# Kernel optimization log

Hardware: AMD Instinct MI355X
Metric: run time of the kernel (lower is better)

Reference implementation:

```python
import jax, jax.numpy as jnp
import numpy as np

B, L, C, H, WS = 8, 1024, 1024, 16, 128  # batch, seq (grid 32x32), dim, heads, window_size
HD = C // H


def _local_mask(seq_len, window_size):
    # blocked where |i - j| > window_size // 2 (matches create_local_attention_mask)
    idx = jnp.arange(seq_len)
    return jnp.abs(idx[:, None] - idx[None, :]) > window_size // 2  # True = blocked


def setup_inputs() -> dict:
    key = jax.random.key(0)
    k0, k1, k2 = jax.random.split(key, 3)
    x = jax.random.normal(k0, (B, L, C), jnp.float32)
    in_proj_w = jax.random.normal(k1, (3 * C, C), jnp.float32) * 0.02
    in_proj_b = jnp.zeros((3 * C,), jnp.float32)
    out_w = jax.random.normal(k2, (C, C), jnp.float32) * 0.02
    out_b = jnp.zeros((C,), jnp.float32)
    return {"x": x, "in_proj_w": in_proj_w, "in_proj_b": in_proj_b,
            "out_w": out_w, "out_b": out_b}


def reference(x, in_proj_w, in_proj_b, out_w, out_b):
    # nn.MultiheadAttention (batch_first, self-attention) with boolean attn_mask.
    Bc, Lc, Cc = x.shape
    qkv = x @ in_proj_w.T + in_proj_b              # [B, L, 3C]
    q, k, v = jnp.split(qkv, 3, axis=-1)
    to_heads = lambda t: t.reshape(Bc, Lc, H, HD).transpose(0, 2, 1, 3)  # [B,H,L,hd]
    q, k, v = to_heads(q), to_heads(k), to_heads(v)
    scale = 1.0 / np.sqrt(HD).astype(np.float32)
    scores = jnp.einsum('bhqd,bhkd->bhqk', q, k) * scale  # [B,H,L,L]
    blocked = _local_mask(Lc, WS)
    scores = jnp.where(blocked[None, None], -jnp.inf, scores)
    attn = jax.nn.softmax(scores, axis=-1)
    out = jnp.einsum('bhqk,bhkd->bhqd', attn, v)           # [B,H,L,hd]
    out = out.transpose(0, 2, 1, 3).reshape(Bc, Lc, Cc)
    return out @ out_w.T + out_b
```

## Files before the change

### kernel.cpp

```cpp
#include <hip/hip_runtime.h>
#include <hip/hip_bf16.h>
#include <stdint.h>


typedef __attribute__((ext_vector_type(8))) short bf16x8;
typedef __attribute__((ext_vector_type(4))) float f32x4;

__device__ inline unsigned short f2b(float f) {
    __hip_bfloat16 h = __float2bfloat16(f);
    return *reinterpret_cast<unsigned short*>(&h);
}

__device__ inline void gld16(const unsigned short* g, unsigned short* l) {
    __builtin_amdgcn_global_load_lds(
        (const __attribute__((address_space(1))) void*)g,
        (__attribute__((address_space(3))) void*)l, 16, 0, 0);
}

#define BM 128
#define BN 128
#define BK 64

__global__ void __launch_bounds__(256) cast_inputs(
    const float4* __restrict__ x, const float4* __restrict__ w1,
    const float4* __restrict__ w2,
    uint4* __restrict__ xb, uint4* __restrict__ w1b, uint4* __restrict__ w2b)
{
    const int P0 = 1048576, P1 = 393216, P2 = 131072;
    int stride = gridDim.x * blockDim.x;
    for (int i = blockIdx.x * blockDim.x + threadIdx.x; i < P0 + P1 + P2; i += stride) {
        const float4* src; uint4* dst; int idx;
        if (i < P0)           { src = x;  dst = xb;  idx = i; }
        else if (i < P0 + P1) { src = w1; dst = w1b; idx = i - P0; }
        else                  { src = w2; dst = w2b; idx = i - P0 - P1; }
        float4 a = src[idx * 2], b = src[idx * 2 + 1];
        unsigned short t[8] = {f2b(a.x), f2b(a.y), f2b(a.z), f2b(a.w),
                               f2b(b.x), f2b(b.y), f2b(b.z), f2b(b.w)};
        dst[idx] = *(uint4*)t;
    }
}

__global__ void __launch_bounds__(256) gemm_qkv(
    const unsigned short* __restrict__ A,
    const unsigned short* __restrict__ W,
    const float* __restrict__ bias,
    unsigned short* __restrict__ Qo,
    unsigned short* __restrict__ Ko,
    unsigned short* __restrict__ Vo)
{
    const int K = 1024;
    int n0 = blockIdx.x * BN;
    int m0 = blockIdx.y * BM;
    int tid = threadIdx.x;
    int wave = tid >> 6, lane = tid & 63;
    int lm = lane & 15, quad = lane >> 4;
    int mblk = (wave & 1) * 64, nblk = (wave >> 1) * 64;

    __shared__ unsigned short As[BM * BK];
    __shared__ unsigned short Bs[BN * BK];

    int drow = lane >> 3;
    int gcc  = (lane & 7) ^ drow;
    const unsigned short* ga[4]; const unsigned short* gb[4];
    unsigned short *la[4], *lb[4];
#pragma unroll
    for (int p = 0; p < 4; ++p) {
        int r = wave * 32 + p * 8 + drow;
        ga[p] = A + (size_t)(m0 + r) * K + gcc * 8;
        gb[p] = W + (size_t)(n0 + r) * K + gcc * 8;
        la[p] = As + (wave * 32 + p * 8) * 64;
        lb[p] = Bs + (wave * 32 + p * 8) * 64;
    }
    int lm7 = lm & 7;

    f32x4 acc[4][4];
#pragma unroll
    for (int i = 0; i < 4; ++i)
#pragma unroll
        for (int j = 0; j < 4; ++j)
            acc[i][j] = (f32x4){0.f, 0.f, 0.f, 0.f};

    for (int k0 = 0; k0 < K; k0 += BK) {
        __syncthreads();
#pragma unroll
        for (int p = 0; p < 4; ++p) gld16(ga[p] + k0, la[p]);
#pragma unroll
        for (int p = 0; p < 4; ++p) gld16(gb[p] + k0, lb[p]);
        __syncthreads();
        bf16x8 af[4][2], bfr[4][2];
#pragma unroll
        for (int i = 0; i < 4; ++i)
#pragma unroll
            for (int hhh = 0; hhh < 2; ++hhh)
                af[i][hhh] = *(const bf16x8*)(As + (mblk + i * 16 + lm) * 64 +
                                              (((hhh * 4 + quad) ^ lm7) << 3));
#pragma unroll
        for (int j = 0; j < 4; ++j)
#pragma unroll
            for (int hhh = 0; hhh < 2; ++hhh)
                bfr[j][hhh] = *(const bf16x8*)(Bs + (nblk + j * 16 + lm) * 64 +
                                               (((hhh * 4 + quad) ^ lm7) << 3));
#pragma unroll
        for (int i = 0; i < 4; ++i)
#pragma unroll
            for (int j = 0; j < 4; ++j) {
                acc[i][j] = __builtin_amdgcn_mfma_f32_16x16x32_bf16(af[i][0], bfr[j][0], acc[i][j], 0, 0, 0);
                acc[i][j] = __builtin_amdgcn_mfma_f32_16x16x32_bf16(af[i][1], bfr[j][1], acc[i][j], 0, 0, 0);
            }
    }

#pragma unroll
    for (int j = 0; j < 4; ++j) {
        int n = n0 + nblk + j * 16 + lm;
        float bv = bias[n];
        int sec = n >> 10, rem = n & 1023;
        int h = rem >> 6, d = rem & 63;
        unsigned short* dst = (sec == 0) ? Qo : (sec == 1) ? Ko : Vo;
#pragma unroll
        for (int i = 0; i < 4; ++i) {
#pragma unroll
            for (int r = 0; r < 4; ++r) {
                int m = m0 + mblk + i * 16 + quad * 4 + r;
                int bb = m >> 10, sl = m & 1023;
                size_t idx = ((size_t)((bb * 16 + h) * 1024 + sl)) * 64 + d;
                dst[idx] = f2b(acc[i][j][r] + bv);
            }
        }
    }
}

__global__ void __launch_bounds__(256) attn_local(
    const unsigned short* __restrict__ Qg,
    const unsigned short* __restrict__ Kg,
    const unsigned short* __restrict__ Vg,
    unsigned short* __restrict__ Og)
{
    const int KP = 72;
    const int VP = 200;
    __shared__ unsigned short Ks[192 * KP];
    __shared__ unsigned short Vt[64 * VP];

    int tid = threadIdx.x;
    int wave = tid >> 6, lane = tid & 63;
    int lm = lane & 15, quad = lane >> 4;

    int bh = blockIdx.x >> 4;
    int qt = blockIdx.x & 15;
    int q0 = qt * 64;
    int b = bh >> 4, h = bh & 15;
    const unsigned short* Qbh = Qg + (size_t)bh * 1024 * 64;
    const unsigned short* Kbh = Kg + (size_t)bh * 1024 * 64;
    const unsigned short* Vbh = Vg + (size_t)bh * 1024 * 64;
    int j0 = q0 - 64;

#pragma unroll
    for (int it = 0; it < 6; ++it) {
        int id = it * 256 + tid;
        int r = id >> 3;
        int c = (id & 7) * 8;
        int j = j0 + r;
        uint4 kv, vv;
        kv.x = kv.y = kv.z = kv.w = 0;
        vv = kv;
        if (j >= 0 && j < 1024) {
            kv = *(const uint4*)(Kbh + (size_t)j * 64 + c);
            vv = *(const uint4*)(Vbh + (size_t)j * 64 + c);
        }
        *(uint4*)(Ks + r * KP + c) = kv;
        unsigned short tmp[8];
        *(uint4*)tmp = vv;
#pragma unroll
        for (int e = 0; e < 8; ++e) Vt[(c + e) * VP + r] = tmp[e];
    }
    __syncthreads();

    int qrow = q0 + wave * 16;
    bf16x8 qf0 = *(const bf16x8*)(Qbh + (size_t)(qrow + lm) * 64 + quad * 8);
    bf16x8 qf1 = *(const bf16x8*)(Qbh + (size_t)(qrow + lm) * 64 + 32 + quad * 8);

    f32x4 sc[9];
#pragma unroll
    for (int kt = 0; kt < 9; ++kt) {
        int akt = wave + kt;
        f32x4 a = (f32x4){0.f, 0.f, 0.f, 0.f};
        bf16x8 k0f = *(const bf16x8*)(Ks + (akt * 16 + lm) * KP + quad * 8);
        bf16x8 k1f = *(const bf16x8*)(Ks + (akt * 16 + lm) * KP + 32 + quad * 8);
        a = __builtin_amdgcn_mfma_f32_16x16x32_bf16(qf0, k0f, a, 0, 0, 0);
        a = __builtin_amdgcn_mfma_f32_16x16x32_bf16(qf1, k1f, a, 0, 0, 0);
        sc[kt] = a;
    }

    float mx[4] = {-3e38f, -3e38f, -3e38f, -3e38f};
#pragma unroll
    for (int kt = 0; kt < 9; ++kt) {
        int jg = j0 + (wave + kt) * 16 + lm;
#pragma unroll
        for (int r = 0; r < 4; ++r) {
            int irow = q0 + wave * 16 + quad * 4 + r;
            int diff = irow - jg;
            bool ok = (jg >= 0) && (jg < 1024) && (diff <= 64) && (diff >= -64);
            float s = ok ? sc[kt][r] * 0.125f : -30000.0f;
            sc[kt][r] = s;
            mx[r] = fmaxf(mx[r], s);
        }
    }
#pragma unroll
    for (int off = 1; off <= 8; off <<= 1)
#pragma unroll
        for (int r = 0; r < 4; ++r)
            mx[r] = fmaxf(mx[r], __shfl_xor(mx[r], off, 64));

    float sum[4] = {0.f, 0.f, 0.f, 0.f};
#pragma unroll
    for (int kt = 0; kt < 9; ++kt)
#pragma unroll
        for (int r = 0; r < 4; ++r) {
            float p = __expf(sc[kt][r] - mx[r]);
            sc[kt][r] = p;
            sum[r] += p;
        }
#pragma unroll
    for (int off = 1; off <= 8; off <<= 1)
#pragma unroll
        for (int r = 0; r < 4; ++r)
            sum[r] += __shfl_xor(sum[r], off, 64);

    __syncthreads();
    unsigned short* Pb = Ks + wave * 3200;
#pragma unroll
    for (int kt = 0; kt < 9; ++kt) {
        int akt = wave + kt;
#pragma unroll
        for (int r = 0; r < 4; ++r)
            Pb[(quad * 4 + r) * VP + akt * 16 + lm] = f2b(sc[kt][r]);
    }
    {
        int zkt = (wave & 1) ? (wave - 1) : (wave + 9);
#pragma unroll
        for (int r = 0; r < 4; ++r)
            Pb[(quad * 4 + r) * VP + zkt * 16 + lm] = 0;
    }
    __syncthreads();

    int jclo = wave >> 1;
    f32x4 o[4];
#pragma unroll
    for (int n = 0; n < 4; ++n) o[n] = (f32x4){0.f, 0.f, 0.f, 0.f};
#pragma unroll
    for (int jc2 = 0; jc2 < 5; ++jc2) {
        int jc = jclo + jc2;
        bf16x8 pf = *(const bf16x8*)(Pb + lm * VP + jc * 32 + quad * 8);
#pragma unroll
        for (int n = 0; n < 4; ++n) {
            bf16x8 vf = *(const bf16x8*)(Vt + (n * 16 + lm) * VP + jc * 32 + quad * 8);
            o[n] = __builtin_amdgcn_mfma_f32_16x16x32_bf16(pf, vf, o[n], 0, 0, 0);
        }
    }

    float inv[4];
#pragma unroll
    for (int r = 0; r < 4; ++r) inv[r] = 1.0f / sum[r];
#pragma unroll
    for (int n = 0; n < 4; ++n)
#pragma unroll
        for (int r = 0; r < 4; ++r) {
            int orow = q0 + wave * 16 + quad * 4 + r;
            size_t oidx = ((size_t)(b * 1024 + orow)) * 1024 + h * 64 + n * 16 + lm;
            Og[oidx] = f2b(o[n][r] * inv[r]);
        }
}

__global__ void __launch_bounds__(256) gemm_proj(
    const unsigned short* __restrict__ A,
    const unsigned short* __restrict__ W,
    const float* __restrict__ bias,
    float* __restrict__ Out)
{
    const int K = 1024;
    int n0 = blockIdx.x * BN;
    int m0 = blockIdx.y * BM;
    int tid = threadIdx.x;
    int wave = tid >> 6, lane = tid & 63;
    int lm = lane & 15, quad = lane >> 4;
    int mblk = (wave & 1) * 64, nblk = (wave >> 1) * 64;

    __shared__ unsigned short As[BM * BK];
    __shared__ unsigned short Bs[BN * BK];

    int drow = lane >> 3;
    int gcc  = (lane & 7) ^ drow;
    const unsigned short* ga[4]; const unsigned short* gb[4];
    unsigned short *la[4], *lb[4];
#pragma unroll
    for (int p = 0; p < 4; ++p) {
        int r = wave * 32 + p * 8 + drow;
        ga[p] = A + (size_t)(m0 + r) * K + gcc * 8;
        gb[p] = W + (size_t)(n0 + r) * K + gcc * 8;
        la[p] = As + (wave * 32 + p * 8) * 64;
        lb[p] = Bs + (wave * 32 + p * 8) * 64;
    }
    int lm7 = lm & 7;

    f32x4 acc[4][4];
#pragma unroll
    for (int i = 0; i < 4; ++i)
#pragma unroll
        for (int j = 0; j < 4; ++j)
            acc[i][j] = (f32x4){0.f, 0.f, 0.f, 0.f};

    for (int k0 = 0; k0 < K; k0 += BK) {
        __syncthreads();
#pragma unroll
        for (int p = 0; p < 4; ++p) gld16(ga[p] + k0, la[p]);
#pragma unroll
        for (int p = 0; p < 4; ++p) gld16(gb[p] + k0, lb[p]);
        __syncthreads();
        bf16x8 af[4][2], bfr[4][2];
#pragma unroll
        for (int i = 0; i < 4; ++i)
#pragma unroll
            for (int hhh = 0; hhh < 2; ++hhh)
                af[i][hhh] = *(const bf16x8*)(As + (mblk + i * 16 + lm) * 64 +
                                              (((hhh * 4 + quad) ^ lm7) << 3));
#pragma unroll
        for (int j = 0; j < 4; ++j)
#pragma unroll
            for (int hhh = 0; hhh < 2; ++hhh)
                bfr[j][hhh] = *(const bf16x8*)(Bs + (nblk + j * 16 + lm) * 64 +
                                               (((hhh * 4 + quad) ^ lm7) << 3));
#pragma unroll
        for (int i = 0; i < 4; ++i)
#pragma unroll
            for (int j = 0; j < 4; ++j) {
                acc[i][j] = __builtin_amdgcn_mfma_f32_16x16x32_bf16(af[i][0], bfr[j][0], acc[i][j], 0, 0, 0);
                acc[i][j] = __builtin_amdgcn_mfma_f32_16x16x32_bf16(af[i][1], bfr[j][1], acc[i][j], 0, 0, 0);
            }
    }

#pragma unroll
    for (int j = 0; j < 4; ++j) {
        int n = n0 + nblk + j * 16 + lm;
        float bv = bias[n];
#pragma unroll
        for (int i = 0; i < 4; ++i) {
#pragma unroll
            for (int r = 0; r < 4; ++r) {
                int m = m0 + mblk + i * 16 + quad * 4 + r;
                Out[(size_t)m * 1024 + n] = acc[i][j][r] + bv;
            }
        }
    }
}

extern "C" void kernel_launch(void* const* d_in, const int* in_sizes, int n_in,
                              void* d_out, int out_size, void* d_ws, size_t ws_size,
                              hipStream_t stream) {
    const float* x  = (const float*)d_in[0];
    const float* w1 = (const float*)d_in[1];
    const float* b1 = (const float*)d_in[2];
    const float* w2 = (const float*)d_in[3];
    const float* b2 = (const float*)d_in[4];
    float* out = (float*)d_out;

    char* ws = (char*)d_ws;
    const size_t MB = 1024 * 1024;
    unsigned short* xb   = (unsigned short*)(ws);
    unsigned short* w1b  = (unsigned short*)(ws + 16 * MB);
    unsigned short* w2b  = (unsigned short*)(ws + 22 * MB);
    unsigned short* q    = (unsigned short*)(ws + 24 * MB);
    unsigned short* k    = (unsigned short*)(ws + 40 * MB);
    unsigned short* v    = (unsigned short*)d_out;
    unsigned short* attn = (unsigned short*)(ws);

    dim3 blk(256);
    cast_inputs<<<1536, blk, 0, stream>>>(
        (const float4*)x, (const float4*)w1, (const float4*)w2,
        (uint4*)xb, (uint4*)w1b, (uint4*)w2b);
    gemm_qkv<<<dim3(24, 64), blk, 0, stream>>>(xb, w1b, b1, q, k, v);
    attn_local<<<dim3(2048), blk, 0, stream>>>(q, k, v, attn);
    gemm_proj<<<dim3(8, 64), blk, 0, stream>>>(attn, w2b, b2, out);
}
```

Measured before the change: 210.0 us.

## Replace QKV and projection GEMMs with 8-wave double-buffered ping-pong GEMM template

```diff
diff --git a/kernel.cpp b/kernel.cpp
--- a/kernel.cpp
+++ b/kernel.cpp
@@ -16,10 +16,6 @@
         (const __attribute__((address_space(1))) void*)g,
         (__attribute__((address_space(3))) void*)l, 16, 0, 0);
 }
-
-#define BM 128
-#define BN 128
-#define BK 64
 
 __global__ void __launch_bounds__(256) cast_inputs(
     const float4* __restrict__ x, const float4* __restrict__ w1,
@@ -40,90 +36,167 @@
     }
 }
 
-__global__ void __launch_bounds__(256) gemm_qkv(
+
+#define STAGE_A(BUF, HM, T) do {                                              \
+    const int rbA = (HM) * 128 + wave * 8;                                    \
+    gld16(Aeff + (size_t)(rbA + drow) * 1024 + (T) * 64 + gcc * 8,            \
+          &As[BUF][rbA * 64]);                                                \
+    gld16(Aeff + (size_t)(rbA + 64 + drow) * 1024 + (T) * 64 + gcc * 8,       \
+          &As[BUF][(rbA + 64) * 64]);                                         \
+} while (0)
+
+#define STAGE_B(BUF, HN, T) do {                                              \
+    const int rbB = (HN) * (BN_T / 2) + wave * 8;                             \
+    gld16(Weff + (size_t)(rbB + drow) * 1024 + (T) * 64 + gcc * 8,            \
+          &Bs[BUF][rbB * 64]);                                                \
+    if constexpr (BN_T == 256) {                                              \
+        gld16(Weff + (size_t)(rbB + 64 + drow) * 1024 + (T) * 64 + gcc * 8,   \
+              &Bs[BUF][(rbB + 64) * 64]);                                     \
+    }                                                                         \
+} while (0)
+
+#define PH_READS(BUF, QM, QN) do {                                            \
+    _Pragma("unroll")                                                         \
+    for (int f = 0; f < 4; ++f) {                                             \
+        const int ar = ((QM) * 128 + f * 32 + wm * 16 + lm) * 64;             \
+        pa[f][0] = *(const bf16x8*)&As[BUF][ar + ((quad ^ lm7) << 3)];        \
+        pa[f][1] = *(const bf16x8*)&As[BUF][ar + (((4 + quad) ^ lm7) << 3)];  \
+    }                                                                         \
+    _Pragma("unroll")                                                         \
+    for (int g = 0; g < NGQ; ++g) {                                           \
+        const int br = (((QN) * NGQ + g) * 64 + wn * 16 + lm) * 64;           \
+        pb[g][0] = *(const bf16x8*)&Bs[BUF][br + ((quad ^ lm7) << 3)];        \
+        pb[g][1] = *(const bf16x8*)&Bs[BUF][br + (((4 + quad) ^ lm7) << 3)];  \
+    }                                                                         \
+} while (0)
+
+#define PH_MMA(QM, QN) do {                                                   \
+    __builtin_amdgcn_s_barrier();                                             \
+    asm volatile("s_waitcnt lgkmcnt(0)" ::: "memory");                        \
+    __builtin_amdgcn_sched_barrier(0);                                        \
+    __builtin_amdgcn_s_setprio(1);                                            \
+    _Pragma("unroll")                                                         \
+    for (int f = 0; f < 4; ++f) {                                             \
+        _Pragma("unroll")                                                     \
+        for (int g = 0; g < NGQ; ++g) {                                       \
+            acc[(QM)*4+f][(QN)*NGQ+g] = __builtin_amdgcn_mfma_f32_16x16x32_bf16( \
+                pa[f][0], pb[g][0], acc[(QM)*4+f][(QN)*NGQ+g], 0, 0, 0);      \
+            acc[(QM)*4+f][(QN)*NGQ+g] = __builtin_amdgcn_mfma_f32_16x16x32_bf16( \
+                pa[f][1], pb[g][1], acc[(QM)*4+f][(QN)*NGQ+g], 0, 0, 0);      \
+        }                                                                     \
+    }                                                                         \
+    __builtin_amdgcn_s_setprio(0);                                            \
+    __builtin_amdgcn_s_barrier();                                             \
+} while (0)
+
+#define VM_WAIT_STEADY do {                                                   \
+    if constexpr (BN_T == 256) { asm volatile("s_waitcnt vmcnt(4)" ::: "memory"); } \
+    else                       { asm volatile("s_waitcnt vmcnt(3)" ::: "memory"); } \
+} while (0)
+
+#define GROUP(BUF, T) do {                                                    \
+    PH_READS(BUF, 0, 0); if ((T) + 1 < NT) STAGE_A((BUF)^1, 1, (T)+1); PH_MMA(0, 0); \
+    PH_READS(BUF, 1, 0); if ((T) + 1 < NT) STAGE_B((BUF)^1, 1, (T)+1); PH_MMA(1, 0); \
+    PH_READS(BUF, 0, 1); if ((T) + 2 < NT) STAGE_B(BUF, 0, (T)+2);     PH_MMA(0, 1); \
+    PH_READS(BUF, 1, 1); if ((T) + 2 < NT) STAGE_A(BUF, 0, (T)+2);            \
+    if ((T) + 2 < NT) { VM_WAIT_STEADY; }                                     \
+    else { asm volatile("s_waitcnt vmcnt(0)" ::: "memory"); }                 \
+    PH_MMA(1, 1);                                                             \
+} while (0)
+
+template<int BN_T, bool SCATTER>
+__global__ void __launch_bounds__(512) gemm8p(
     const unsigned short* __restrict__ A,
     const unsigned short* __restrict__ W,
     const float* __restrict__ bias,
     unsigned short* __restrict__ Qo,
     unsigned short* __restrict__ Ko,
-    unsigned short* __restrict__ Vo)
+    unsigned short* __restrict__ Vo,
+    float* __restrict__ Out)
 {
-    const int K = 1024;
-    int n0 = blockIdx.x * BN;
-    int m0 = blockIdx.y * BM;
-    int tid = threadIdx.x;
-    int wave = tid >> 6, lane = tid & 63;
-    int lm = lane & 15, quad = lane >> 4;
-    int mblk = (wave & 1) * 64, nblk = (wave >> 1) * 64;
-
-    __shared__ unsigned short As[BM * BK];
-    __shared__ unsigned short Bs[BN * BK];
-
-    int drow = lane >> 3;
-    int gcc  = (lane & 7) ^ drow;
-    const unsigned short* ga[4]; const unsigned short* gb[4];
-    unsigned short *la[4], *lb[4];
-#pragma unroll
-    for (int p = 0; p < 4; ++p) {
-        int r = wave * 32 + p * 8 + drow;
-        ga[p] = A + (size_t)(m0 + r) * K + gcc * 8;
-        gb[p] = W + (size_t)(n0 + r) * K + gcc * 8;
-        la[p] = As + (wave * 32 + p * 8) * 64;
-        lb[p] = Bs + (wave * 32 + p * 8) * 64;
-    }
-    int lm7 = lm & 7;
-
-    f32x4 acc[4][4];
-#pragma unroll
-    for (int i = 0; i < 4; ++i)
-#pragma unroll
-        for (int j = 0; j < 4; ++j)
-            acc[i][j] = (f32x4){0.f, 0.f, 0.f, 0.f};
-
-    for (int k0 = 0; k0 < K; k0 += BK) {
-        __syncthreads();
-#pragma unroll
-        for (int p = 0; p < 4; ++p) gld16(ga[p] + k0, la[p]);
-#pragma unroll
-        for (int p = 0; p < 4; ++p) gld16(gb[p] + k0, lb[p]);
-        __syncthreads();
-        bf16x8 af[4][2], bfr[4][2];
-#pragma unroll
-        for (int i = 0; i < 4; ++i)
-#pragma unroll
-            for (int hhh = 0; hhh < 2; ++hhh)
-                af[i][hhh] = *(const bf16x8*)(As + (mblk + i * 16 + lm) * 64 +
-                                              (((hhh * 4 + quad) ^ lm7) << 3));
-#pragma unroll
-        for (int j = 0; j < 4; ++j)
-#pragma unroll
-            for (int hhh = 0; hhh < 2; ++hhh)
-                bfr[j][hhh] = *(const bf16x8*)(Bs + (nblk + j * 16 + lm) * 64 +
-                                               (((hhh * 4 + quad) ^ lm7) << 3));
-#pragma unroll
-        for (int i = 0; i < 4; ++i)
-#pragma unroll
-            for (int j = 0; j < 4; ++j) {
-                acc[i][j] = __builtin_amdgcn_mfma_f32_16x16x32_bf16(af[i][0], bfr[j][0], acc[i][j], 0, 0, 0);
-                acc[i][j] = __builtin_amdgcn_mfma_f32_16x16x32_bf16(af[i][1], bfr[j][1], acc[i][j], 0, 0, 0);
+    constexpr int NT  = 16;
+    constexpr int NFN = BN_T / 64;
+    constexpr int NGQ = NFN / 2;
+    constexpr int NDIM = SCATTER ? 3072 : 1024;
+    constexpr int NBX = NDIM / BN_T;
+    constexpr int QC  = (NBX * 32) / 8;
+
+    __shared__ unsigned short As[2][256 * 64];
+    __shared__ unsigned short Bs[2][BN_T * 64];
+
+    const int tid  = threadIdx.x;
+    const int wave = tid >> 6, lane = tid & 63;
+    const int wm = wave >> 2, wn = wave & 3;
+    const int lm = lane & 15, quad = lane >> 4;
+    const int lm7 = lm & 7;
+    const int drow = lane >> 3;
+    const int gcc  = (lane & 7) ^ drow;
+
+    const int id  = blockIdx.y * NBX + blockIdx.x;
+    const int swz = (id & 7) * QC + (id >> 3);
+    const int bx = swz % NBX, by = swz / NBX;
+    const int m0 = by * 256, n0 = bx * BN_T;
+
+    const unsigned short* Aeff = A + (size_t)m0 * 1024;
+    const unsigned short* Weff = W + (size_t)n0 * 1024;
+
+    f32x4 acc[8][NFN];
+#pragma unroll
+    for (int f = 0; f < 8; ++f)
+#pragma unroll
+        for (int g = 0; g < NFN; ++g)
+            acc[f][g] = (f32x4){0.f, 0.f, 0.f, 0.f};
+
+    bf16x8 pa[4][2];
+    bf16x8 pb[NGQ][2];
+
+    STAGE_A(0, 0, 0);
+    STAGE_A(0, 1, 0);
+    STAGE_B(0, 0, 0);
+    STAGE_B(0, 1, 0);
+    STAGE_B(1, 0, 1);
+    STAGE_A(1, 0, 1);
+    VM_WAIT_STEADY;
+    __builtin_amdgcn_s_barrier();
+
+#pragma unroll 1
+    for (int tp = 0; tp < NT / 2; ++tp) {
+        const int te = 2 * tp;
+        GROUP(0, te);
+        GROUP(1, te + 1);
+    }
+
+    if constexpr (SCATTER) {
+#pragma unroll
+        for (int g = 0; g < NFN; ++g) {
+            int n = n0 + g * 64 + wn * 16 + lm;
+            float bv = bias[n];
+            int sec = n >> 10, rem = n & 1023;
+            int h = rem >> 6, d = rem & 63;
+            unsigned short* dst = (sec == 0) ? Qo : (sec == 1) ? Ko : Vo;
+#pragma unroll
+            for (int f = 0; f < 8; ++f) {
+#pragma unroll
+                for (int r = 0; r < 4; ++r) {
+                    int m = m0 + f * 32 + wm * 16 + quad * 4 + r;
+                    int bb = m >> 10, sl = m & 1023;
+                    size_t idx = ((size_t)((bb * 16 + h) * 1024 + sl)) * 64 + d;
+                    dst[idx] = f2b(acc[f][g][r] + bv);
+                }
             }
-    }
-
-#pragma unroll
-    for (int j = 0; j < 4; ++j) {
-        int n = n0 + nblk + j * 16 + lm;
-        float bv = bias[n];
-        int sec = n >> 10, rem = n & 1023;
-        int h = rem >> 6, d = rem & 63;
-        unsigned short* dst = (sec == 0) ? Qo : (sec == 1) ? Ko : Vo;
-#pragma unroll
-        for (int i = 0; i < 4; ++i) {
-#pragma unroll
-            for (int r = 0; r < 4; ++r) {
-                int m = m0 + mblk + i * 16 + quad * 4 + r;
-                int bb = m >> 10, sl = m & 1023;
-                size_t idx = ((size_t)((bb * 16 + h) * 1024 + sl)) * 64 + d;
-                dst[idx] = f2b(acc[i][j][r] + bv);
+        }
+    } else {
+#pragma unroll
+        for (int g = 0; g < NFN; ++g) {
+            int n = n0 + g * 64 + wn * 16 + lm;
+            float bv = bias[n];
+#pragma unroll
+            for (int f = 0; f < 8; ++f) {
+#pragma unroll
+                for (int r = 0; r < 4; ++r) {
+                    int m = m0 + f * 32 + wm * 16 + quad * 4 + r;
+                    Out[(size_t)m * 1024 + n] = acc[f][g][r] + bv;
+                }
             }
         }
     }
@@ -270,88 +343,6 @@
         }
 }
 
-__global__ void __launch_bounds__(256) gemm_proj(
-    const unsigned short* __restrict__ A,
-    const unsigned short* __restrict__ W,
-    const float* __restrict__ bias,
-    float* __restrict__ Out)
-{
-    const int K = 1024;
-    int n0 = blockIdx.x * BN;
-    int m0 = blockIdx.y * BM;
-    int tid = threadIdx.x;
-    int wave = tid >> 6, lane = tid & 63;
-    int lm = lane & 15, quad = lane >> 4;
-    int mblk = (wave & 1) * 64, nblk = (wave >> 1) * 64;
-
-    __shared__ unsigned short As[BM * BK];
-    __shared__ unsigned short Bs[BN * BK];
-
-    int drow = lane >> 3;
-    int gcc  = (lane & 7) ^ drow;
-    const unsigned short* ga[4]; const unsigned short* gb[4];
-    unsigned short *la[4], *lb[4];
-#pragma unroll
-    for (int p = 0; p < 4; ++p) {
-        int r = wave * 32 + p * 8 + drow;
-        ga[p] = A + (size_t)(m0 + r) * K + gcc * 8;
-        gb[p] = W + (size_t)(n0 + r) * K + gcc * 8;
-        la[p] = As + (wave * 32 + p * 8) * 64;
-        lb[p] = Bs + (wave * 32 + p * 8) * 64;
-    }
-    int lm7 = lm & 7;
-
-    f32x4 acc[4][4];
-#pragma unroll
-    for (int i = 0; i < 4; ++i)
-#pragma unroll
-        for (int j = 0; j < 4; ++j)
-            acc[i][j] = (f32x4){0.f, 0.f, 0.f, 0.f};
-
-    for (int k0 = 0; k0 < K; k0 += BK) {
-        __syncthreads();
-#pragma unroll
-        for (int p = 0; p < 4; ++p) gld16(ga[p] + k0, la[p]);
-#pragma unroll
-        for (int p = 0; p < 4; ++p) gld16(gb[p] + k0, lb[p]);
-        __syncthreads();
-        bf16x8 af[4][2], bfr[4][2];
-#pragma unroll
-        for (int i = 0; i < 4; ++i)
-#pragma unroll
-            for (int hhh = 0; hhh < 2; ++hhh)
-                af[i][hhh] = *(const bf16x8*)(As + (mblk + i * 16 + lm) * 64 +
-                                              (((hhh * 4 + quad) ^ lm7) << 3));
-#pragma unroll
-        for (int j = 0; j < 4; ++j)
-#pragma unroll
-            for (int hhh = 0; hhh < 2; ++hhh)
-                bfr[j][hhh] = *(const bf16x8*)(Bs + (nblk + j * 16 + lm) * 64 +
-                                               (((hhh * 4 + quad) ^ lm7) << 3));
-#pragma unroll
-        for (int i = 0; i < 4; ++i)
-#pragma unroll
-            for (int j = 0; j < 4; ++j) {
-                acc[i][j] = __builtin_amdgcn_mfma_f32_16x16x32_bf16(af[i][0], bfr[j][0], acc[i][j], 0, 0, 0);
-                acc[i][j] = __builtin_amdgcn_mfma_f32_16x16x32_bf16(af[i][1], bfr[j][1], acc[i][j], 0, 0, 0);
-            }
-    }
-
-#pragma unroll
-    for (int j = 0; j < 4; ++j) {
-        int n = n0 + nblk + j * 16 + lm;
-        float bv = bias[n];
-#pragma unroll
-        for (int i = 0; i < 4; ++i) {
-#pragma unroll
-            for (int r = 0; r < 4; ++r) {
-                int m = m0 + mblk + i * 16 + quad * 4 + r;
-                Out[(size_t)m * 1024 + n] = acc[i][j][r] + bv;
-            }
-        }
-    }
-}
-
 extern "C" void kernel_launch(void* const* d_in, const int* in_sizes, int n_in,
                               void* d_out, int out_size, void* d_ws, size_t ws_size,
                               hipStream_t stream) {
@@ -372,11 +363,12 @@
     unsigned short* v    = (unsigned short*)d_out;
     unsigned short* attn = (unsigned short*)(ws);
 
-    dim3 blk(256);
-    cast_inputs<<<1536, blk, 0, stream>>>(
+    cast_inputs<<<1536, dim3(256), 0, stream>>>(
         (const float4*)x, (const float4*)w1, (const float4*)w2,
         (uint4*)xb, (uint4*)w1b, (uint4*)w2b);
-    gemm_qkv<<<dim3(24, 64), blk, 0, stream>>>(xb, w1b, b1, q, k, v);
-    attn_local<<<dim3(2048), blk, 0, stream>>>(q, k, v, attn);
-    gemm_proj<<<dim3(8, 64), blk, 0, stream>>>(attn, w2b, b2, out);
-}
+    gemm8p<256, true><<<dim3(12, 32), dim3(512), 0, stream>>>(
+        xb, w1b, b1, q, k, v, nullptr);
+    attn_local<<<dim3(2048), dim3(256), 0, stream>>>(q, k, v, attn);
+    gemm8p<128, false><<<dim3(8, 32), dim3(512), 0, stream>>>(
+        attn, w2b, b2, nullptr, nullptr, nullptr, out);
+}
```

New measurement: 235.7 us. 12.2% more time.

## Double-buffer GEMM LDS tiles, prefetch next tile during MFMA, add XCD workgroup swizzle

Applied to the files above, without the earlier changes.

```diff
diff --git a/kernel.cpp b/kernel.cpp
--- a/kernel.cpp
+++ b/kernel.cpp
@@ -40,36 +40,83 @@
     }
 }
 
-__global__ void __launch_bounds__(256) gemm_qkv(
+
+#define STG(BUF, T) do {                                                      \
+    _Pragma("unroll")                                                         \
+    for (int p = 0; p < 4; ++p) {                                             \
+        gld16(ga[p] + (T) * 64, &As[BUF][(wave * 32 + p * 8) * 64]);          \
+        gld16(gb[p] + (T) * 64, &Bs[BUF][(wave * 32 + p * 8) * 64]);          \
+    } } while (0)
+
+#define RDS(BUF) do {                                                         \
+    _Pragma("unroll")                                                         \
+    for (int i = 0; i < 4; ++i) {                                             \
+        _Pragma("unroll")                                                     \
+        for (int h = 0; h < 2; ++h) {                                         \
+            af[i][h]  = *(const bf16x8*)&As[BUF][(mblk + i * 16 + lm) * 64 +  \
+                                                 (((h * 4 + quad) ^ lm7) << 3)]; \
+            bfr[i][h] = *(const bf16x8*)&Bs[BUF][(nblk + i * 16 + lm) * 64 +  \
+                                                 (((h * 4 + quad) ^ lm7) << 3)]; \
+        }                                                                     \
+    } } while (0)
+
+#define MMA do {                                                              \
+    asm volatile("s_waitcnt lgkmcnt(0)" ::: "memory");                        \
+    __builtin_amdgcn_sched_barrier(0);                                        \
+    _Pragma("unroll")                                                         \
+    for (int i = 0; i < 4; ++i) {                                             \
+        _Pragma("unroll")                                                     \
+        for (int j = 0; j < 4; ++j) {                                         \
+            acc[i][j] = __builtin_amdgcn_mfma_f32_16x16x32_bf16(              \
+                af[i][0], bfr[j][0], acc[i][j], 0, 0, 0);                     \
+            acc[i][j] = __builtin_amdgcn_mfma_f32_16x16x32_bf16(              \
+                af[i][1], bfr[j][1], acc[i][j], 0, 0, 0);                     \
+        }                                                                     \
+    } } while (0)
+
+#define ITER(BUF, T) do {                                                     \
+    RDS(BUF);                                                                 \
+    STG(1 - (BUF), (T) + 1);                                                  \
+    MMA;                                                                      \
+    asm volatile("s_waitcnt vmcnt(0)" ::: "memory");                          \
+    __builtin_amdgcn_s_barrier();                                             \
+} while (0)
+
+template<bool SCATTER>
+__global__ void __launch_bounds__(256) gemm2p(
     const unsigned short* __restrict__ A,
     const unsigned short* __restrict__ W,
     const float* __restrict__ bias,
     unsigned short* __restrict__ Qo,
     unsigned short* __restrict__ Ko,
-    unsigned short* __restrict__ Vo)
+    unsigned short* __restrict__ Vo,
+    float* __restrict__ Out,
+    int NBX)
 {
     const int K = 1024;
-    int n0 = blockIdx.x * BN;
-    int m0 = blockIdx.y * BM;
     int tid = threadIdx.x;
     int wave = tid >> 6, lane = tid & 63;
     int lm = lane & 15, quad = lane >> 4;
     int mblk = (wave & 1) * 64, nblk = (wave >> 1) * 64;
 
-    __shared__ unsigned short As[BM * BK];
-    __shared__ unsigned short Bs[BN * BK];
+    int nwg = NBX * 64;
+    int id  = blockIdx.y * NBX + blockIdx.x;
+    int cpx = nwg >> 3;
+    int swz = (id & 7) * cpx + (id >> 3);
+    int bx = swz % NBX, by = swz / NBX;
+    int n0 = bx * BN, m0 = by * BM;
+
+    __shared__ unsigned short As[2][BM * BK];
+    __shared__ unsigned short Bs[2][BN * BK];
 
     int drow = lane >> 3;
     int gcc  = (lane & 7) ^ drow;
     const unsigned short* ga[4]; const unsigned short* gb[4];
-    unsigned short *la[4], *lb[4];
 #pragma unroll
     for (int p = 0; p < 4; ++p) {
         int r = wave * 32 + p * 8 + drow;
         ga[p] = A + (size_t)(m0 + r) * K + gcc * 8;
         gb[p] = W + (size_t)(n0 + r) * K + gcc * 8;
-        la[p] = As + (wave * 32 + p * 8) * 64;
-        lb[p] = Bs + (wave * 32 + p * 8) * 64;
     }
     int lm7 = lm & 7;
 
@@ -79,51 +126,52 @@
 #pragma unroll
         for (int j = 0; j < 4; ++j)
             acc[i][j] = (f32x4){0.f, 0.f, 0.f, 0.f};
-
-    for (int k0 = 0; k0 < K; k0 += BK) {
-        __syncthreads();
-#pragma unroll
-        for (int p = 0; p < 4; ++p) gld16(ga[p] + k0, la[p]);
-#pragma unroll
-        for (int p = 0; p < 4; ++p) gld16(gb[p] + k0, lb[p]);
-        __syncthreads();
-        bf16x8 af[4][2], bfr[4][2];
-#pragma unroll
-        for (int i = 0; i < 4; ++i)
-#pragma unroll
-            for (int hhh = 0; hhh < 2; ++hhh)
-                af[i][hhh] = *(const bf16x8*)(As + (mblk + i * 16 + lm) * 64 +
-                                              (((hhh * 4 + quad) ^ lm7) << 3));
-#pragma unroll
-        for (int j = 0; j < 4; ++j)
-#pragma unroll
-            for (int hhh = 0; hhh < 2; ++hhh)
-                bfr[j][hhh] = *(const bf16x8*)(Bs + (nblk + j * 16 + lm) * 64 +
-                                               (((hhh * 4 + quad) ^ lm7) << 3));
-#pragma unroll
-        for (int i = 0; i < 4; ++i)
-#pragma unroll
-            for (int j = 0; j < 4; ++j) {
-                acc[i][j] = __builtin_amdgcn_mfma_f32_16x16x32_bf16(af[i][0], bfr[j][0], acc[i][j], 0, 0, 0);
-                acc[i][j] = __builtin_amdgcn_mfma_f32_16x16x32_bf16(af[i][1], bfr[j][1], acc[i][j], 0, 0, 0);
+    bf16x8 af[4][2], bfr[4][2];
+
+    STG(0, 0);
+    asm volatile("s_waitcnt vmcnt(0)" ::: "memory");
+    __builtin_amdgcn_s_barrier();
+
+#pragma unroll 1
+    for (int tp = 0; tp < 7; ++tp) {
+        ITER(0, 2 * tp);
+        ITER(1, 2 * tp + 1);
+    }
+    ITER(0, 14);
+    RDS(1);
+    MMA;
+
+    if constexpr (SCATTER) {
+#pragma unroll
+        for (int j = 0; j < 4; ++j) {
+            int n = n0 + nblk + j * 16 + lm;
+            float bv = bias[n];
+            int sec = n >> 10, rem = n & 1023;
+            int h = rem >> 6, d = rem & 63;
+            unsigned short* dst = (sec == 0) ? Qo : (sec == 1) ? Ko : Vo;
+#pragma unroll
+            for (int i = 0; i < 4; ++i) {
+#pragma unroll
+                for (int r = 0; r < 4; ++r) {
+                    int m = m0 + mblk + i * 16 + quad * 4 + r;
+                    int bb = m >> 10, sl = m & 1023;
+                    size_t idx = ((size_t)((bb * 16 + h) * 1024 + sl)) * 64 + d;
+                    dst[idx] = f2b(acc[i][j][r] + bv);
+                }
             }
-    }
-
-#pragma unroll
-    for (int j = 0; j < 4; ++j) {
-        int n = n0 + nblk + j * 16 + lm;
-        float bv = bias[n];
-        int sec = n >> 10, rem = n & 1023;
-        int h = rem >> 6, d = rem & 63;
-        unsigned short* dst = (sec == 0) ? Qo : (sec == 1) ? Ko : Vo;
-#pragma unroll
-        for (int i = 0; i < 4; ++i) {
-#pragma unroll
-            for (int r = 0; r < 4; ++r) {
-                int m = m0 + mblk + i * 16 + quad * 4 + r;
-                int bb = m >> 10, sl = m & 1023;
-                size_t idx = ((size_t)((bb * 16 + h) * 1024 + sl)) * 64 + d;
-                dst[idx] = f2b(acc[i][j][r] + bv);
+        }
+    } else {
+#pragma unroll
+        for (int j = 0; j < 4; ++j) {
+            int n = n0 + nblk + j * 16 + lm;
+            float bv = bias[n];
+#pragma unroll
+            for (int i = 0; i < 4; ++i) {
+#pragma unroll
+                for (int r = 0; r < 4; ++r) {
+                    int m = m0 + mblk + i * 16 + quad * 4 + r;
+                    Out[(size_t)m * 1024 + n] = acc[i][j][r] + bv;
+                }
             }
         }
     }
@@ -270,88 +318,6 @@
         }
 }
 
-__global__ void __launch_bounds__(256) gemm_proj(
-    const unsigned short* __restrict__ A,
-    const unsigned short* __restrict__ W,
-    const float* __restrict__ bias,
-    float* __restrict__ Out)
-{
-    const int K = 1024;
-    int n0 = blockIdx.x * BN;
-    int m0 = blockIdx.y * BM;
-    int tid = threadIdx.x;
-    int wave = tid >> 6, lane = tid & 63;
-    int lm = lane & 15, quad = lane >> 4;
-    int mblk = (wave & 1) * 64, nblk = (wave >> 1) * 64;
-
-    __shared__ unsigned short As[BM * BK];
-    __shared__ unsigned short Bs[BN * BK];
-
-    int drow = lane >> 3;
-    int gcc  = (lane & 7) ^ drow;
-    const unsigned short* ga[4]; const unsigned short* gb[4];
-    unsigned short *la[4], *lb[4];
-#pragma unroll
-    for (int p = 0; p < 4; ++p) {
-        int r = wave * 32 + p * 8 + drow;
-        ga[p] = A + (size_t)(m0 + r) * K + gcc * 8;
-        gb[p] = W + (size_t)(n0 + r) * K + gcc * 8;
-        la[p] = As + (wave * 32 + p * 8) * 64;
-        lb[p] = Bs + (wave * 32 + p * 8) * 64;
-    }
-    int lm7 = lm & 7;
-
-    f32x4 acc[4][4];
-#pragma unroll
-    for (int i = 0; i < 4; ++i)
-#pragma unroll
-        for (int j = 0; j < 4; ++j)
-            acc[i][j] = (f32x4){0.f, 0.f, 0.f, 0.f};
-
-    for (int k0 = 0; k0 < K; k0 += BK) {
-        __syncthreads();
-#pragma unroll
-        for (int p = 0; p < 4; ++p) gld16(ga[p] + k0, la[p]);
-#pragma unroll
-        for (int p = 0; p < 4; ++p) gld16(gb[p] + k0, lb[p]);
-        __syncthreads();
-        bf16x8 af[4][2], bfr[4][2];
-#pragma unroll
-        for (int i = 0; i < 4; ++i)
-#pragma unroll
-            for (int hhh = 0; hhh < 2; ++hhh)
-                af[i][hhh] = *(const bf16x8*)(As + (mblk + i * 16 + lm) * 64 +
-                                              (((hhh * 4 + quad) ^ lm7) << 3));
-#pragma unroll
-        for (int j = 0; j < 4; ++j)
-#pragma unroll
-            for (int hhh = 0; hhh < 2; ++hhh)
-                bfr[j][hhh] = *(const bf16x8*)(Bs + (nblk + j * 16 + lm) * 64 +
-                                               (((hhh * 4 + quad) ^ lm7) << 3));
-#pragma unroll
-        for (int i = 0; i < 4; ++i)
-#pragma unroll
-            for (int j = 0; j < 4; ++j) {
-                acc[i][j] = __builtin_amdgcn_mfma_f32_16x16x32_bf16(af[i][0], bfr[j][0], acc[i][j], 0, 0, 0);
-                acc[i][j] = __builtin_amdgcn_mfma_f32_16x16x32_bf16(af[i][1], bfr[j][1], acc[i][j], 0, 0, 0);
-            }
-    }
-
-#pragma unroll
-    for (int j = 0; j < 4; ++j) {
-        int n = n0 + nblk + j * 16 + lm;
-        float bv = bias[n];
-#pragma unroll
-        for (int i = 0; i < 4; ++i) {
-#pragma unroll
-            for (int r = 0; r < 4; ++r) {
-                int m = m0 + mblk + i * 16 + quad * 4 + r;
-                Out[(size_t)m * 1024 + n] = acc[i][j][r] + bv;
-            }
-        }
-    }
-}
-
 extern "C" void kernel_launch(void* const* d_in, const int* in_sizes, int n_in,
                               void* d_out, int out_size, void* d_ws, size_t ws_size,
                               hipStream_t stream) {
@@ -372,11 +338,12 @@
     unsigned short* v    = (unsigned short*)d_out;
     unsigned short* attn = (unsigned short*)(ws);
 
-    dim3 blk(256);
-    cast_inputs<<<1536, blk, 0, stream>>>(
+    cast_inputs<<<1536, dim3(256), 0, stream>>>(
         (const float4*)x, (const float4*)w1, (const float4*)w2,
         (uint4*)xb, (uint4*)w1b, (uint4*)w2b);
-    gemm_qkv<<<dim3(24, 64), blk, 0, stream>>>(xb, w1b, b1, q, k, v);
-    attn_local<<<dim3(2048), blk, 0, stream>>>(q, k, v, attn);
-    gemm_proj<<<dim3(8, 64), blk, 0, stream>>>(attn, w2b, b2, out);
-}
+    gemm2p<true><<<dim3(24, 64), dim3(256), 0, stream>>>(
+        xb, w1b, b1, q, k, v, nullptr, 24);
+    attn_local<<<dim3(2048), dim3(256), 0, stream>>>(q, k, v, attn);
+    gemm2p<false><<<dim3(8, 64), dim3(256), 0, stream>>>(
+        attn, w2b, b2, nullptr, nullptr, nullptr, out, 8);
+}
```

After: 262.2 us. 24.9% more time.
